# Kernel tuning notes

Hardware: AMD Instinct MI355X
Metric: run time of the kernel (lower is better)

The kernel has to match this reference:

```python
import jax, jax.numpy as jnp
import numpy as np
from jax import lax

SINKHORN_ITERS = 20


def sinkhorn_knopp(logits, tau=1.0, iterations=SINKHORN_ITERS):
    # logits: [N, K]. Log-domain alternating row/col normalization.
    N, K = logits.shape
    P = logits / tau
    log_target_col_sum = jnp.log(jnp.asarray(N / K, dtype=logits.dtype) + 1e-9)

    def step(P, _):
        P = P - jax.nn.logsumexp(P, axis=1, keepdims=True)   # row sums -> 1
        P = P - jax.nn.logsumexp(P, axis=0, keepdims=True) + log_target_col_sum  # col sums -> N/K
        return P, None

    P, _ = lax.scan(step, P, None, length=iterations)
    return jnp.exp(P)


def setup_inputs() -> dict:
    key = jax.random.key(0)
    ks = jax.random.split(key, 8)
    N, C, K, B = 200000, 128, 32, 16
    x = jax.random.normal(ks[0], (N, C), dtype=jnp.float32)
    batch = jnp.sort(jax.random.randint(ks[1], (N,), 0, B))
    # assign_mlp: Linear(C,C) -> ReLU -> Linear(C,K)
    W1 = jax.random.normal(ks[2], (C, C), dtype=jnp.float32) / np.sqrt(C)
    b1 = jnp.zeros((C,), dtype=jnp.float32)
    W2 = jax.random.normal(ks[3], (C, K), dtype=jnp.float32) / np.sqrt(C)
    b2 = jnp.zeros((K,), dtype=jnp.float32)
    scaling = jnp.asarray(5.0, dtype=jnp.float32)
    return {"x": x, "batch": batch, "W1": W1, "b1": b1, "W2": W2, "b2": b2,
            "scaling": scaling, "num_graphs": B}


def reference(x, batch, W1, b1, W2, b2, scaling, num_graphs):
    # assignment logits: MLP(x) * scaling  -> [N, K]
    h = jax.nn.relu(x @ W1 + b1)
    logits = (h @ W2 + b2) * scaling
    # doubly-stochastic soft assignment via Sinkhorn-Knopp (tau=1.0, 20 iters)
    s = sinkhorn_knopp(logits, tau=1.0, iterations=SINKHORN_ITERS)  # [N, K]
    # pooled super-node features: scatter-sum over graphs of s[n,k]*x[n,c]
    onehot = jax.nn.one_hot(batch, num_graphs, dtype=x.dtype)        # [N, B]
    out = jnp.einsum('nb,nk,nc->bkc', onehot, s, x)                  # [B, K, C]
    return out
```

## Files before the change

### kernel.cpp

```cpp
#include <hip/hip_runtime.h>
#include <hip/hip_bf16.h>

#define C_DIM 128
#define K_DIM 32
#define N_ITERS 20
#define WPAD 136
#define SK_THREADS 832
#define SK_WAVES 13
#define NGRP 16
#define GSIZE 16

typedef __attribute__((ext_vector_type(8))) short short8;
typedef __attribute__((ext_vector_type(4))) float f32x4;
typedef __attribute__((ext_vector_type(4))) unsigned short us4;

__device__ __forceinline__ unsigned short f2bf(float f) {
    __hip_bfloat16 h = __float2bfloat16(f);
    return *reinterpret_cast<unsigned short*>(&h);
}

__global__ void init_kernel(float* __restrict__ out, int n_out,
                            float* __restrict__ zreg, int n_z,
                            const float* __restrict__ W1, const float* __restrict__ W2,
                            unsigned short* __restrict__ W1t,
                            unsigned short* __restrict__ W2t) {
    int i = blockIdx.x * blockDim.x + threadIdx.x;
    int stride = gridDim.x * blockDim.x;
    for (int j = i; j < n_out; j += stride) out[j] = 0.f;
    for (int j = i; j < n_z; j += stride) zreg[j] = 0.f;
    for (int j = i; j < C_DIM * C_DIM; j += stride) {
        int n = j >> 7, k = j & 127;
        W1t[j] = f2bf(W1[k * C_DIM + n]);
    }
    for (int j = i; j < C_DIM * K_DIM; j += stride) {
        int n = j >> 7, k = j & 127;
        W2t[j] = f2bf(W2[k * K_DIM + n]);
    }
}

__global__ __launch_bounds__(256, 4) void mlp_kernel(
    const float* __restrict__ x, const unsigned short* __restrict__ W1t,
    const float* __restrict__ b1, const unsigned short* __restrict__ W2t,
    const float* __restrict__ b2, const float* __restrict__ scal,
    float* __restrict__ Lg, int N, int ntiles) {
    __shared__ unsigned short sW1[C_DIM][WPAD];
    __shared__ unsigned short sW2[K_DIM][WPAD];
    __shared__ unsigned short sX[64][WPAD];
    __shared__ unsigned short sH[4][16][WPAD];
    __shared__ float sB1[C_DIM];
    __shared__ float sB2[K_DIM];

    const int tid = threadIdx.x;
    for (int i = tid; i < C_DIM * 16; i += 256) {
        const int r = i >> 4, c8 = (i & 15) * 8;
        *(float4*)&sW1[r][c8] = *(const float4*)&W1t[r * C_DIM + c8];
    }
    for (int i = tid; i < K_DIM * 16; i += 256) {
        const int r = i >> 4, c8 = (i & 15) * 8;
        *(float4*)&sW2[r][c8] = *(const float4*)&W2t[r * C_DIM + c8];
    }
    if (tid < C_DIM) sB1[tid] = b1[tid];
    if (tid < K_DIM) sB2[tid] = b2[tid];
    const float sc = *scal;

    const int wave = tid >> 6;
    const int lane = tid & 63;
    const int lr = lane & 15;
    const int kg = lane >> 4;
    __syncthreads();

    for (int tile = blockIdx.x; tile < ntiles; tile += gridDim.x) {
        const int row0 = tile * 64;
        __syncthreads();
        for (int i = tid; i < 2048; i += 256) {
            const int r = i >> 5, c4 = (i & 31) * 4;
            const float4 v = *(const float4*)&x[(size_t)(row0 + r) * C_DIM + c4];
            us4 u;
            u.x = f2bf(v.x); u.y = f2bf(v.y); u.z = f2bf(v.z); u.w = f2bf(v.w);
            *(us4*)&sX[r][c4] = u;
        }
        __syncthreads();

        short8 a[4];
#pragma unroll
        for (int kt = 0; kt < 4; ++kt)
            a[kt] = *(const short8*)&sX[wave * 16 + lr][kt * 32 + kg * 8];
#pragma unroll
        for (int ct = 0; ct < 8; ++ct) {
            const float bv = sB1[ct * 16 + lr];
            f32x4 acc = {bv, bv, bv, bv};
#pragma unroll
            for (int kt = 0; kt < 4; ++kt) {
                const short8 b = *(const short8*)&sW1[ct * 16 + lr][kt * 32 + kg * 8];
                acc = __builtin_amdgcn_mfma_f32_16x16x32_bf16(a[kt], b, acc, 0, 0, 0);
            }
#pragma unroll
            for (int r = 0; r < 4; ++r)
                sH[wave][kg * 4 + r][ct * 16 + lr] = f2bf(fmaxf(acc[r], 0.f));
        }
        __syncthreads();

        short8 a2[4];
#pragma unroll
        for (int kt = 0; kt < 4; ++kt)
            a2[kt] = *(const short8*)&sH[wave][lr][kt * 32 + kg * 8];
#pragma unroll
        for (int ct = 0; ct < 2; ++ct) {
            const float bv = sB2[ct * 16 + lr];
            f32x4 acc = {bv, bv, bv, bv};
#pragma unroll
            for (int kt = 0; kt < 4; ++kt) {
                const short8 b = *(const short8*)&sW2[ct * 16 + lr][kt * 32 + kg * 8];
                acc = __builtin_amdgcn_mfma_f32_16x16x32_bf16(a2[kt], b, acc, 0, 0, 0);
            }
#pragma unroll
            for (int r = 0; r < 4; ++r) {
                const int g = row0 + wave * 16 + kg * 4 + r;
                Lg[(size_t)g * K_DIM + ct * 16 + lr] = acc[r] * sc;
            }
        }
    }
}

__device__ __forceinline__ int bitrev5(int l) {
    return ((l & 1) << 4) | ((l & 2) << 2) | (l & 4) | ((l & 8) >> 2) |
           ((l & 16) >> 4);
}

#define FOLD_STAGE(M, HALF)                                   \
    {                                                         \
        const bool hi = (lane & (M)) != 0;                    \
        _Pragma("unroll")                                     \
        for (int j = 0; j < (HALF); ++j) {                    \
            const float give = hi ? p[j] : p[j + (HALF)];     \
            const float keep = hi ? p[j + (HALF)] : p[j];     \
            p[j] = keep + __shfl_xor(give, (M));              \
        }                                                     \
    }

__global__ __launch_bounds__(SK_THREADS) void sinkhorn_kernel(
    float* __restrict__ Lg, float* __restrict__ shards, float* __restrict__ vglob,
    int* __restrict__ garr, int* __restrict__ rarr, int* __restrict__ done,
    int* __restrict__ gdone, int N) {
    __shared__ float sv[K_DIM];
    __shared__ float sw[K_DIM];
    __shared__ float swsd[K_DIM];
    __shared__ float swsum[SK_WAVES][K_DIM];
    const int tid = threadIdx.x;
    const int wave = tid >> 6;
    const int lane = tid & 63;
    const int g = blockIdx.x >> 4;
    const size_t n = (size_t)blockIdx.x * SK_THREADS + tid;
    const bool valid = n < (size_t)N;
    const float log_tgt = __logf((float)N / (float)K_DIM);

    if (tid < K_DIM) { sv[tid] = 0.f; sw[tid] = 1.f; }

    float E[K_DIM];
    if (valid) {
        const float4* Lr = (const float4*)(Lg + n * K_DIM);
#pragma unroll
        for (int j = 0; j < 8; ++j) {
            const float4 v = Lr[j];
            E[4 * j] = v.x; E[4 * j + 1] = v.y; E[4 * j + 2] = v.z; E[4 * j + 3] = v.w;
        }
        float M = E[0];
#pragma unroll
        for (int j = 1; j < K_DIM; ++j) M = fmaxf(M, E[j]);
#pragma unroll
        for (int j = 0; j < K_DIM; ++j) E[j] = __expf(E[j] - M);
    } else {
#pragma unroll
        for (int j = 0; j < K_DIM; ++j) E[j] = 0.f;
    }
    __syncthreads();

    float r_last = 0.f;
    for (int t = 1; t <= N_ITERS; ++t) {
        float up = 0.f;
#pragma unroll
        for (int j = 0; j < K_DIM; ++j) up = fmaf(E[j], sw[j], up);
        float r = 0.f;
        if (valid) r = 1.0f / up;
        r_last = r;
        float p[K_DIM];
#pragma unroll
        for (int j = 0; j < K_DIM; ++j) p[j] = E[j] * r;

        FOLD_STAGE(1, 16)
        FOLD_STAGE(2, 8)
        FOLD_STAGE(4, 4)
        FOLD_STAGE(8, 2)
        FOLD_STAGE(16, 1)
        const float tot = p[0] + __shfl_xor(p[0], 32);
        if (lane < K_DIM) swsum[wave][bitrev5(lane)] = tot;
        __syncthreads();

        if (wave == 0) {
            if (lane < K_DIM) {
                float s_ = 0.f;
#pragma unroll
                for (int w = 0; w < SK_WAVES; ++w) s_ += swsum[w][lane];
                atomicAdd(&shards[((size_t)t * NGRP + g) * K_DIM + lane], s_);
            }
            asm volatile("s_waitcnt vmcnt(0)" ::: "memory");
            int is_gl = 0, is_rl = 0;
            if (lane == 0) {
                const int ga = __hip_atomic_fetch_add(&garr[t * NGRP + g], 1,
                                                      __ATOMIC_RELAXED,
                                                      __HIP_MEMORY_SCOPE_AGENT);
                is_gl = (ga == GSIZE - 1);
                if (is_gl) {
                    const int ra = __hip_atomic_fetch_add(&rarr[t], 1,
                                                          __ATOMIC_RELAXED,
                                                          __HIP_MEMORY_SCOPE_AGENT);
                    is_rl = (ra == NGRP - 1);
                }
            }
            is_gl = __shfl(is_gl, 0);
            is_rl = __shfl(is_rl, 0);
            if (is_rl) {
                if (lane < K_DIM) {
                    float cs = 0.f;
#pragma unroll
                    for (int gg = 0; gg < NGRP; ++gg)
                        cs += __hip_atomic_load(
                            &shards[((size_t)t * NGRP + gg) * K_DIM + lane],
                            __ATOMIC_RELAXED, __HIP_MEMORY_SCOPE_AGENT);
                    cs *= sw[lane];
                    const float v = (t < N_ITERS) ? (__logf(cs) - log_tgt)
                                                  : ((float)N / (float)K_DIM) / cs;
                    __hip_atomic_store(&vglob[t * K_DIM + lane], v,
                                       __ATOMIC_RELAXED, __HIP_MEMORY_SCOPE_AGENT);
                }
                asm volatile("s_waitcnt vmcnt(0)" ::: "memory");
                if (lane == 0) {
                    __hip_atomic_store(done + t, 1, __ATOMIC_RELAXED,
                                       __HIP_MEMORY_SCOPE_AGENT);
                    __hip_atomic_store(&gdone[t * NGRP + g], 1, __ATOMIC_RELAXED,
                                       __HIP_MEMORY_SCOPE_AGENT);
                }
            } else if (is_gl) {
                if (lane == 0) {
                    while (__hip_atomic_load(done + t, __ATOMIC_RELAXED,
                                             __HIP_MEMORY_SCOPE_AGENT) == 0)
                        __builtin_amdgcn_s_sleep(1);
                    __hip_atomic_store(&gdone[t * NGRP + g], 1, __ATOMIC_RELAXED,
                                       __HIP_MEMORY_SCOPE_AGENT);
                }
            } else {
                if (lane == 0) {
                    while (__hip_atomic_load(&gdone[t * NGRP + g], __ATOMIC_RELAXED,
                                             __HIP_MEMORY_SCOPE_AGENT) == 0)
                        __builtin_amdgcn_s_sleep(1);
                }
            }
            if (lane < K_DIM) {
                const float v = __hip_atomic_load(&vglob[t * K_DIM + lane],
                                                  __ATOMIC_RELAXED,
                                                  __HIP_MEMORY_SCOPE_AGENT);
                if (t < N_ITERS) {
                    sv[lane] += v;
                    sw[lane] = __expf(-sv[lane]);
                } else {
                    swsd[lane] = sw[lane] * v;
                }
            }
        }
        __syncthreads();
    }

    if (valid) {
        float4* Sr = (float4*)(Lg + n * K_DIM);
#pragma unroll
        for (int j = 0; j < 8; ++j) {
            float4 o;
            o.x = E[4 * j + 0] * swsd[4 * j + 0] * r_last;
            o.y = E[4 * j + 1] * swsd[4 * j + 1] * r_last;
            o.z = E[4 * j + 2] * swsd[4 * j + 2] * r_last;
            o.w = E[4 * j + 3] * swsd[4 * j + 3] * r_last;
            Sr[j] = o;
        }
    }
}

#define PCHUNK 96
#define PCH_PER_BLOCK 4

__global__ __launch_bounds__(256) void pool_kernel(
    const float* __restrict__ x, const int* __restrict__ batch,
    const float* __restrict__ Sg, float* __restrict__ out, int N) {
    __shared__ float sx[PCHUNK][C_DIM];
    __shared__ float ss[PCHUNK][K_DIM];
    __shared__ int sb[PCHUNK];

    const int tid = threadIdx.x;
    const int k0 = (tid >> 5) * 4;
    const int c0 = (tid & 31) * 4;
    float acc[4][4];
#pragma unroll
    for (int i = 0; i < 4; ++i)
#pragma unroll
        for (int j = 0; j < 4; ++j) acc[i][j] = 0.f;

    int cur_b = -1;
    const int base0 = blockIdx.x * (PCHUNK * PCH_PER_BLOCK);

    for (int cc = 0; cc < PCH_PER_BLOCK; ++cc) {
        const int base = base0 + cc * PCHUNK;
        if (base >= N) break;
        const int rows = min(PCHUNK, N - base);
        __syncthreads();
        {
            const float4* src = (const float4*)(x + (size_t)base * C_DIM);
            for (int i = tid; i < rows * (C_DIM / 4); i += 256)
                ((float4*)&sx[0][0])[i] = src[i];
            const float4* ssrc = (const float4*)(Sg + (size_t)base * K_DIM);
            for (int i = tid; i < rows * (K_DIM / 4); i += 256)
                ((float4*)&ss[0][0])[i] = ssrc[i];
        }
        if (tid < rows) sb[tid] = batch[base + tid];
        __syncthreads();

        for (int r = 0; r < rows; ++r) {
            const int b = sb[r];
            if (b != cur_b) {
                if (cur_b >= 0) {
                    float* ob = out + ((size_t)cur_b * K_DIM + k0) * C_DIM + c0;
#pragma unroll
                    for (int i = 0; i < 4; ++i)
#pragma unroll
                        for (int j = 0; j < 4; ++j) {
                            atomicAdd(&ob[i * C_DIM + j], acc[i][j]);
                            acc[i][j] = 0.f;
                        }
                }
                cur_b = b;
            }
            const float4 sv = *(const float4*)&ss[r][k0];
            const float4 xv = *(const float4*)&sx[r][c0];
            const float sA[4] = {sv.x, sv.y, sv.z, sv.w};
            const float xA[4] = {xv.x, xv.y, xv.z, xv.w};
#pragma unroll
            for (int i = 0; i < 4; ++i)
#pragma unroll
                for (int j = 0; j < 4; ++j)
                    acc[i][j] = fmaf(sA[i], xA[j], acc[i][j]);
        }
    }
    if (cur_b >= 0) {
        float* ob = out + ((size_t)cur_b * K_DIM + k0) * C_DIM + c0;
#pragma unroll
        for (int i = 0; i < 4; ++i)
#pragma unroll
            for (int j = 0; j < 4; ++j) atomicAdd(&ob[i * C_DIM + j], acc[i][j]);
    }
}

extern "C" void kernel_launch(void* const* d_in, const int* in_sizes, int n_in,
                              void* d_out, int out_size, void* d_ws, size_t ws_size,
                              hipStream_t stream) {
    const float* x = (const float*)d_in[0];
    const int* batch = (const int*)d_in[1];
    const float* W1 = (const float*)d_in[2];
    const float* b1 = (const float*)d_in[3];
    const float* W2 = (const float*)d_in[4];
    const float* b2 = (const float*)d_in[5];
    const float* scal = (const float*)d_in[6];
    float* out = (float*)d_out;

    const int N = in_sizes[1];

    float* Lg = (float*)d_ws;
    float* shards = Lg + (size_t)N * K_DIM;
    const int n_shard_f = (N_ITERS + 1) * NGRP * K_DIM;
    float* vglob = shards + n_shard_f;
    const int n_vglob = (N_ITERS + 1) * K_DIM;
    int* garr = (int*)(vglob + n_vglob);
    int* rarr = garr + 352;
    int* done = rarr + 32;
    int* gdone = done + 32;
    unsigned short* W1t = (unsigned short*)(gdone + 352);
    unsigned short* W2t = W1t + C_DIM * C_DIM;
    const int n_z = n_shard_f + n_vglob + 352 + 32 + 32 + 352;

    init_kernel<<<64, 256, 0, stream>>>(out, out_size, shards, n_z,
                                        W1, W2, W1t, W2t);

    const int ntiles = N / 64;
    mlp_kernel<<<640, 256, 0, stream>>>(x, W1t, b1, W2t, b2, scal, Lg, N, ntiles);

    const int sblocks = NGRP * GSIZE;
    sinkhorn_kernel<<<sblocks, SK_THREADS, 0, stream>>>(Lg, shards, vglob,
                                                        garr, rarr, done, gdone, N);

    const int pblocks = (N + PCHUNK * PCH_PER_BLOCK - 1) / (PCHUNK * PCH_PER_BLOCK);
    pool_kernel<<<pblocks, 256, 0, stream>>>(x, batch, Lg, out, N);
}
```

Measured before the change: 496.9 us.

## Load x directly into MFMA registers, split Sinkhorn into two launches, retune grids

The MLP kernel drops the shared-memory staging of x. Each wave now loads its fp32 rows straight from global memory and packs them to bf16 with v_cvt_pk_bf16_f32, which removes two block barriers per tile. Occupancy hints and grid sizes change for the MLP and pool kernels. The Sinkhorn kernel is split into two launches of ten iterations each, carrying the column potentials through a global buffer, so the exp and row reload are done twice in exchange for a shorter persistent spin loop.

```diff
diff --git a/kernel.cpp b/kernel.cpp
--- a/kernel.cpp
+++ b/kernel.cpp
@@ -12,11 +12,25 @@
 
 typedef __attribute__((ext_vector_type(8))) short short8;
 typedef __attribute__((ext_vector_type(4))) float f32x4;
-typedef __attribute__((ext_vector_type(4))) unsigned short us4;
 
 __device__ __forceinline__ unsigned short f2bf(float f) {
     __hip_bfloat16 h = __float2bfloat16(f);
     return *reinterpret_cast<unsigned short*>(&h);
+}
+
+__device__ __forceinline__ unsigned short f2bf_fast(float f) {
+    unsigned int u;
+    asm("v_cvt_pk_bf16_f32 %0, %1, %1" : "=v"(u) : "v"(f));
+    return (unsigned short)u;
+}
+
+__device__ __forceinline__ short8 pack8(float4 q0, float4 q1) {
+    union { unsigned int u[4]; short8 s; } cv;
+    asm("v_cvt_pk_bf16_f32 %0, %1, %2" : "=v"(cv.u[0]) : "v"(q0.x), "v"(q0.y));
+    asm("v_cvt_pk_bf16_f32 %0, %1, %2" : "=v"(cv.u[1]) : "v"(q0.z), "v"(q0.w));
+    asm("v_cvt_pk_bf16_f32 %0, %1, %2" : "=v"(cv.u[2]) : "v"(q1.x), "v"(q1.y));
+    asm("v_cvt_pk_bf16_f32 %0, %1, %2" : "=v"(cv.u[3]) : "v"(q1.z), "v"(q1.w));
+    return cv.s;
 }
 
 __global__ void init_kernel(float* __restrict__ out, int n_out,
@@ -38,14 +52,13 @@
     }
 }
 
-__global__ __launch_bounds__(256, 4) void mlp_kernel(
+__global__ __launch_bounds__(256, 2) void mlp_kernel(
     const float* __restrict__ x, const unsigned short* __restrict__ W1t,
     const float* __restrict__ b1, const unsigned short* __restrict__ W2t,
     const float* __restrict__ b2, const float* __restrict__ scal,
     float* __restrict__ Lg, int N, int ntiles) {
     __shared__ unsigned short sW1[C_DIM][WPAD];
     __shared__ unsigned short sW2[K_DIM][WPAD];
-    __shared__ unsigned short sX[64][WPAD];
     __shared__ unsigned short sH[4][16][WPAD];
     __shared__ float sB1[C_DIM];
     __shared__ float sB2[K_DIM];
@@ -71,20 +84,15 @@
 
     for (int tile = blockIdx.x; tile < ntiles; tile += gridDim.x) {
         const int row0 = tile * 64;
-        __syncthreads();
-        for (int i = tid; i < 2048; i += 256) {
-            const int r = i >> 5, c4 = (i & 31) * 4;
-            const float4 v = *(const float4*)&x[(size_t)(row0 + r) * C_DIM + c4];
-            us4 u;
-            u.x = f2bf(v.x); u.y = f2bf(v.y); u.z = f2bf(v.z); u.w = f2bf(v.w);
-            *(us4*)&sX[r][c4] = u;
-        }
-        __syncthreads();
-
+
+        const float* xr = x + (size_t)(row0 + wave * 16 + lr) * C_DIM + kg * 8;
         short8 a[4];
 #pragma unroll
-        for (int kt = 0; kt < 4; ++kt)
-            a[kt] = *(const short8*)&sX[wave * 16 + lr][kt * 32 + kg * 8];
+        for (int kt = 0; kt < 4; ++kt) {
+            const float4 q0 = *(const float4*)(xr + kt * 32);
+            const float4 q1 = *(const float4*)(xr + kt * 32 + 4);
+            a[kt] = pack8(q0, q1);
+        }
 #pragma unroll
         for (int ct = 0; ct < 8; ++ct) {
             const float bv = sB1[ct * 16 + lr];
@@ -96,9 +104,8 @@
             }
 #pragma unroll
             for (int r = 0; r < 4; ++r)
-                sH[wave][kg * 4 + r][ct * 16 + lr] = f2bf(fmaxf(acc[r], 0.f));
-        }
-        __syncthreads();
+                sH[wave][kg * 4 + r][ct * 16 + lr] = f2bf_fast(fmaxf(acc[r], 0.f));
+        }
 
         short8 a2[4];
 #pragma unroll
@@ -141,7 +148,7 @@
 __global__ __launch_bounds__(SK_THREADS) void sinkhorn_kernel(
     float* __restrict__ Lg, float* __restrict__ shards, float* __restrict__ vglob,
     int* __restrict__ garr, int* __restrict__ rarr, int* __restrict__ done,
-    int* __restrict__ gdone, int N) {
+    int* __restrict__ gdone, float* __restrict__ svbuf, int N, int tb, int te) {
     __shared__ float sv[K_DIM];
     __shared__ float sw[K_DIM];
     __shared__ float swsd[K_DIM];
@@ -154,7 +161,11 @@
     const bool valid = n < (size_t)N;
     const float log_tgt = __logf((float)N / (float)K_DIM);
 
-    if (tid < K_DIM) { sv[tid] = 0.f; sw[tid] = 1.f; }
+    if (tid < K_DIM) {
+        const float v0 = (tb == 1) ? 0.f : svbuf[tid];
+        sv[tid] = v0;
+        sw[tid] = __expf(-v0);
+    }
 
     float E[K_DIM];
     if (valid) {
@@ -176,7 +187,7 @@
     __syncthreads();
 
     float r_last = 0.f;
-    for (int t = 1; t <= N_ITERS; ++t) {
+    for (int t = tb; t <= te; ++t) {
         float up = 0.f;
 #pragma unroll
         for (int j = 0; j < K_DIM; ++j) up = fmaf(E[j], sw[j], up);
@@ -270,6 +281,11 @@
         __syncthreads();
     }
 
+    if (te < N_ITERS) {
+        if (wave == 0 && lane < K_DIM) svbuf[lane] = sv[lane];
+        return;
+    }
+
     if (valid) {
         float4* Sr = (float4*)(Lg + n * K_DIM);
 #pragma unroll
@@ -285,7 +301,7 @@
 }
 
 #define PCHUNK 96
-#define PCH_PER_BLOCK 4
+#define PCH_PER_BLOCK 2
 
 __global__ __launch_bounds__(256) void pool_kernel(
     const float* __restrict__ x, const int* __restrict__ batch,
@@ -380,19 +396,22 @@
     int* rarr = garr + 352;
     int* done = rarr + 32;
     int* gdone = done + 32;
-    unsigned short* W1t = (unsigned short*)(gdone + 352);
+    float* svbuf = (float*)(gdone + 352);
+    unsigned short* W1t = (unsigned short*)(svbuf + 32);
     unsigned short* W2t = W1t + C_DIM * C_DIM;
-    const int n_z = n_shard_f + n_vglob + 352 + 32 + 32 + 352;
+    const int n_z = n_shard_f + n_vglob + 352 + 32 + 32 + 352 + 32;
 
     init_kernel<<<64, 256, 0, stream>>>(out, out_size, shards, n_z,
                                         W1, W2, W1t, W2t);
 
     const int ntiles = N / 64;
-    mlp_kernel<<<640, 256, 0, stream>>>(x, W1t, b1, W2t, b2, scal, Lg, N, ntiles);
+    mlp_kernel<<<768, 256, 0, stream>>>(x, W1t, b1, W2t, b2, scal, Lg, N, ntiles);
 
     const int sblocks = NGRP * GSIZE;
-    sinkhorn_kernel<<<sblocks, SK_THREADS, 0, stream>>>(Lg, shards, vglob,
-                                                        garr, rarr, done, gdone, N);
+    sinkhorn_kernel<<<sblocks, SK_THREADS, 0, stream>>>(
+        Lg, shards, vglob, garr, rarr, done, gdone, svbuf, N, 1, 10);
+    sinkhorn_kernel<<<sblocks, SK_THREADS, 0, stream>>>(
+        Lg, shards, vglob, garr, rarr, done, gdone, svbuf, N, 11, 20);
 
     const int pblocks = (N + PCHUNK * PCH_PER_BLOCK - 1) / (PCHUNK * PCH_PER_BLOCK);
     pool_kernel<<<pblocks, 256, 0, stream>>>(x, batch, Lg, out, N);
```

Measured after the change: 476.9 us. 4.0% less time.
